# Optimization experiments

Hardware: AMD Instinct MI355X
Metric: run time of the kernel (lower is better)

Reference implementation:

```python
import jax, jax.numpy as jnp
import numpy as np


def setup_inputs() -> dict:
    key = jax.random.key(0)
    k1, k2, k3, k4 = jax.random.split(key, 4)
    B, T, K, N = 8, 16, 4096, 16384
    x = jax.random.normal(k1, (B, T, K), dtype=jnp.float32)
    # int8 weights in [-127, 127]
    weight_int8 = jax.random.randint(k2, (N, K), -127, 128, dtype=jnp.int32).astype(jnp.int8)
    # row-wise absmax scales (positive)
    weight_scales = jax.random.uniform(k3, (N,), dtype=jnp.float32, minval=0.1, maxval=2.0)
    bias = jax.random.normal(k4, (N,), dtype=jnp.float32)
    return {"x": x, "weight_int8": weight_int8, "weight_scales": weight_scales, "bias": bias}


def reference(x, weight_int8, weight_scales, bias):
    # dequantize_rowwise: W_fp = int8 * (scale / 127) per output row
    w = weight_int8.astype(x.dtype) * (weight_scales / 127.0).astype(x.dtype)[:, None]  # [N, K]
    # F.linear(x, w, bias) = x @ w.T + bias
    out = jnp.einsum('btk,nk->btn', x, w) + bias
    return out
```

## Files before the change

kernel.cpp:

```cpp
#include <hip/hip_runtime.h>
#include <hip/hip_bf16.h>

typedef __attribute__((ext_vector_type(8))) short short8;
typedef __attribute__((ext_vector_type(4))) float f32x4;
typedef __attribute__((ext_vector_type(4))) int   i32x4;

#define KD 4096
#define ND 16384
#define MD 128

__device__ __forceinline__ ushort f2bf_rn(float f) {
    unsigned u = __float_as_uint(f);
    u += 0x7FFFu + ((u >> 16) & 1u);
    return (ushort)(u >> 16);
}

__device__ __forceinline__ ushort i2bf(int v) {
    return (ushort)(__float_as_uint((float)v) >> 16);
}

__global__ __launch_bounds__(256) void pack_x_kernel(const float* __restrict__ x,
                                                     ushort* __restrict__ xp) {
    int tid  = blockIdx.x * 256 + threadIdx.x;
    int lane = tid & 63;
    int mt   = (tid >> 6) & 7;
    int kb   = tid >> 9;
    int m = (mt << 4) + (lane & 15);
    int k = (kb << 5) + ((lane >> 4) << 3);
    const f32x4* src = reinterpret_cast<const f32x4*>(x + (size_t)m * KD + k);
    f32x4 a = src[0];
    f32x4 b = src[1];
    short8 v;
    v[0] = (short)f2bf_rn(a[0]); v[1] = (short)f2bf_rn(a[1]);
    v[2] = (short)f2bf_rn(a[2]); v[3] = (short)f2bf_rn(a[3]);
    v[4] = (short)f2bf_rn(b[0]); v[5] = (short)f2bf_rn(b[1]);
    v[6] = (short)f2bf_rn(b[2]); v[7] = (short)f2bf_rn(b[3]);
    *reinterpret_cast<short8*>(xp + (size_t)tid * 8) = v;
}

#define GLOAD_LDS16(g, l)                                                        \
    __builtin_amdgcn_global_load_lds((const __attribute__((address_space(1))) void*)(g), \
                                     (__attribute__((address_space(3))) void*)(l), 16, 0, 0)

__global__ __launch_bounds__(512) void gemm_kernel(const int* __restrict__ wgt,
                                                   const ushort* __restrict__ xp,
                                                   const float* __restrict__ scales,
                                                   const float* __restrict__ bias,
                                                   float* __restrict__ out) {
    __shared__ __align__(16) char lds[98304];

    const int tid  = threadIdx.x;
    const int lane = tid & 63;
    const int w    = tid >> 6;
    const int n0   = blockIdx.x << 6;
    const int cl   = lane & 15;
    const int cq   = lane >> 4;

    if (w >= 4) {
        const int p = w - 4;
        const char* asrc = (const char*)xp + (p << 12) + (lane << 4);
        const int* wsrc0;
        const int* wsrc1;
        const int* wsrc2;
        const int* wsrc3;
        {
            int c0 = (p << 4) + 0  + cq;
            int c1 = (p << 4) + 4  + cq;
            int c2 = (p << 4) + 8  + cq;
            int c3 = (p << 4) + 12 + cq;
            wsrc0 = wgt + (size_t)(n0 + c0) * KD + ((cl ^ (c0 & 7)) << 2);
            wsrc1 = wgt + (size_t)(n0 + c1) * KD + ((cl ^ (c1 & 7)) << 2);
            wsrc2 = wgt + (size_t)(n0 + c2) * KD + ((cl ^ (c2 & 7)) << 2);
            wsrc3 = wgt + (size_t)(n0 + c3) * KD + ((cl ^ (c3 & 7)) << 2);
        }
        char* dA = lds + (p << 12);
        char* dW = lds + 49152 + (p << 12);

#define STAGE(t, b) do {                                                        \
            const char* _as = asrc + (size_t)(t) * 16384;                       \
            char* _dA = dA + (b) * 16384;                                       \
            GLOAD_LDS16(_as,        _dA);                                       \
            GLOAD_LDS16(_as + 1024, _dA + 1024);                                \
            GLOAD_LDS16(_as + 2048, _dA + 2048);                                \
            GLOAD_LDS16(_as + 3072, _dA + 3072);                                \
            const int _k0 = (t) * 64;                                           \
            char* _dW = dW + (b) * 16384;                                       \
            GLOAD_LDS16(wsrc0 + _k0, _dW);                                      \
            GLOAD_LDS16(wsrc1 + _k0, _dW + 1024);                               \
            GLOAD_LDS16(wsrc2 + _k0, _dW + 2048);                               \
            GLOAD_LDS16(wsrc3 + _k0, _dW + 3072);                               \
        } while (0)

        STAGE(0, 0);
        STAGE(1, 1);
        asm volatile("s_waitcnt vmcnt(8)" ::: "memory");
        __builtin_amdgcn_s_barrier();

        int b2 = 2;
#pragma unroll 1
        for (int t = 0; t < 64; ++t) {
            if (t + 2 < 64) {
                STAGE(t + 2, b2);
                asm volatile("s_waitcnt vmcnt(8)" ::: "memory");
            } else if (t + 1 < 64) {
                asm volatile("s_waitcnt vmcnt(0)" ::: "memory");
            }
            __builtin_amdgcn_s_barrier();
            b2 = (b2 == 2) ? 0 : b2 + 1;
        }
#undef STAGE
        return;
    }

    f32x4 acc[8];
#pragma unroll
    for (int i = 0; i < 8; ++i) acc[i] = (f32x4){0.f, 0.f, 0.f, 0.f};

    const char* rA = lds + (lane << 4);
    const char* rW = lds + 49152 + (((w << 4) + cl) << 8);
    const unsigned sw  = (unsigned)((cl & 7) << 4);
    const unsigned q32 = (unsigned)(cq << 5);

    __syncthreads();

    int bc = 0;
#pragma unroll 1
    for (int t = 0; t < 64; ++t) {
        const char* wb = rW + bc * 16384;
        const char* ab = rA + bc * 16384;
#pragma unroll
        for (int j = 0; j < 2; ++j) {
            unsigned off = (unsigned)((j << 7) + q32) ^ sw;
            i32x4 lo = *reinterpret_cast<const i32x4*>(wb + off);
            i32x4 hi = *reinterpret_cast<const i32x4*>(wb + (off ^ 16u));
            short8 bf;
            bf[0] = (short)i2bf(lo[0]); bf[1] = (short)i2bf(lo[1]);
            bf[2] = (short)i2bf(lo[2]); bf[3] = (short)i2bf(lo[3]);
            bf[4] = (short)i2bf(hi[0]); bf[5] = (short)i2bf(hi[1]);
            bf[6] = (short)i2bf(hi[2]); bf[7] = (short)i2bf(hi[3]);
            const char* aj = ab + j * 8192;
#pragma unroll
            for (int mt = 0; mt < 8; ++mt) {
                short8 af = *reinterpret_cast<const short8*>(aj + mt * 1024);
                acc[mt] = __builtin_amdgcn_mfma_f32_16x16x32_bf16(af, bf, acc[mt], 0, 0, 0);
            }
        }
        __syncthreads();
        bc = (bc == 2) ? 0 : bc + 1;
    }

    const int ncol = n0 + (w << 4) + cl;
    const float s  = scales[ncol] * (1.0f / 127.0f);
    const float bv = bias[ncol];
    const int rb = cq << 2;
#pragma unroll
    for (int mt = 0; mt < 8; ++mt) {
#pragma unroll
        for (int r = 0; r < 4; ++r) {
            int mg = (mt << 4) + rb + r;
            out[(size_t)mg * ND + ncol] = acc[mt][r] * s + bv;
        }
    }
}

extern "C" void kernel_launch(void* const* d_in, const int* in_sizes, int n_in,
                              void* d_out, int out_size, void* d_ws, size_t ws_size,
                              hipStream_t stream) {
    const float* x      = (const float*)d_in[0];
    const int*   wgt    = (const int*)d_in[1];
    const float* scales = (const float*)d_in[2];
    const float* bias   = (const float*)d_in[3];
    float* out = (float*)d_out;
    ushort* xp = (ushort*)d_ws;

    pack_x_kernel<<<MD * KD / (8 * 256), 256, 0, stream>>>(x, xp);
    gemm_kernel<<<256, 512, 0, stream>>>(wgt, xp, scales, bias, out);
}
```

Before: 57.77 us.

## Read activations directly from global memory and stage only weights through LDS

Producer waves now stage only weight tiles into LDS, using a K-tile twice as deep (128 ints per row, 32 iterations instead of 64) that fills the whole triple-buffered LDS region. Compute waves load the packed bf16 activation fragments straight from global memory, relying on the small activation buffer staying cache-resident. The aim is to halve producer load traffic and barrier count per K and give weight streaming the full LDS budget. In exchange, compute waves now wait on global or cache latency for activations with no prefetch, and the four compute waves each reload the same activation data.

```diff
diff --git a/kernel.cpp b/kernel.cpp
--- a/kernel.cpp
+++ b/kernel.cpp
@@ -58,37 +58,21 @@
 
     if (w >= 4) {
         const int p = w - 4;
-        const char* asrc = (const char*)xp + (p << 12) + (lane << 4);
-        const int* wsrc0;
-        const int* wsrc1;
-        const int* wsrc2;
-        const int* wsrc3;
-        {
-            int c0 = (p << 4) + 0  + cq;
-            int c1 = (p << 4) + 4  + cq;
-            int c2 = (p << 4) + 8  + cq;
-            int c3 = (p << 4) + 12 + cq;
-            wsrc0 = wgt + (size_t)(n0 + c0) * KD + ((cl ^ (c0 & 7)) << 2);
-            wsrc1 = wgt + (size_t)(n0 + c1) * KD + ((cl ^ (c1 & 7)) << 2);
-            wsrc2 = wgt + (size_t)(n0 + c2) * KD + ((cl ^ (c2 & 7)) << 2);
-            wsrc3 = wgt + (size_t)(n0 + c3) * KD + ((cl ^ (c3 & 7)) << 2);
+        const int* wsrc[8];
+#pragma unroll
+        for (int i = 0; i < 8; ++i) {
+            int c = (p << 4) + (i << 1) + (lane >> 5);
+            int k = ((lane & 31) << 2) ^ ((c & 7) << 2);
+            wsrc[i] = wgt + (size_t)(n0 + c) * KD + k;
         }
-        char* dA = lds + (p << 12);
-        char* dW = lds + 49152 + (p << 12);
+        char* dW = lds + (p << 13);
 
 #define STAGE(t, b) do {                                                        \
-            const char* _as = asrc + (size_t)(t) * 16384;                       \
-            char* _dA = dA + (b) * 16384;                                       \
-            GLOAD_LDS16(_as,        _dA);                                       \
-            GLOAD_LDS16(_as + 1024, _dA + 1024);                                \
-            GLOAD_LDS16(_as + 2048, _dA + 2048);                                \
-            GLOAD_LDS16(_as + 3072, _dA + 3072);                                \
-            const int _k0 = (t) * 64;                                           \
-            char* _dW = dW + (b) * 16384;                                       \
-            GLOAD_LDS16(wsrc0 + _k0, _dW);                                      \
-            GLOAD_LDS16(wsrc1 + _k0, _dW + 1024);                               \
-            GLOAD_LDS16(wsrc2 + _k0, _dW + 2048);                               \
-            GLOAD_LDS16(wsrc3 + _k0, _dW + 3072);                               \
+            const int _k0 = (t) * 128;                                          \
+            char* _d = dW + (b) * 32768;                                        \
+            _Pragma("unroll")                                                   \
+            for (int _i = 0; _i < 8; ++_i)                                      \
+                GLOAD_LDS16(wsrc[_i] + _k0, _d + _i * 1024);                    \
         } while (0)
 
         STAGE(0, 0);
@@ -98,11 +82,11 @@
 
         int b2 = 2;
 #pragma unroll 1
-        for (int t = 0; t < 64; ++t) {
-            if (t + 2 < 64) {
+        for (int t = 0; t < 32; ++t) {
+            if (t + 2 < 32) {
                 STAGE(t + 2, b2);
                 asm volatile("s_waitcnt vmcnt(8)" ::: "memory");
-            } else if (t + 1 < 64) {
+            } else if (t + 1 < 32) {
                 asm volatile("s_waitcnt vmcnt(0)" ::: "memory");
             }
             __builtin_amdgcn_s_barrier();
@@ -116,20 +100,25 @@
 #pragma unroll
     for (int i = 0; i < 8; ++i) acc[i] = (f32x4){0.f, 0.f, 0.f, 0.f};
 
-    const char* rA = lds + (lane << 4);
-    const char* rW = lds + 49152 + (((w << 4) + cl) << 8);
+    const char* rW = lds + (((w << 4) + cl) << 9);
     const unsigned sw  = (unsigned)((cl & 7) << 4);
     const unsigned q32 = (unsigned)(cq << 5);
+    const char* ax = (const char*)xp + (lane << 4);
 
     __syncthreads();
 
     int bc = 0;
 #pragma unroll 1
-    for (int t = 0; t < 64; ++t) {
-        const char* wb = rW + bc * 16384;
-        const char* ab = rA + bc * 16384;
+    for (int t = 0; t < 32; ++t) {
+        const char* wb = rW + bc * 32768;
+        const char* at = ax + (size_t)t * 32768;
 #pragma unroll
-        for (int j = 0; j < 2; ++j) {
+        for (int j = 0; j < 4; ++j) {
+            short8 af[8];
+            const char* aj = at + j * 8192;
+#pragma unroll
+            for (int mt = 0; mt < 8; ++mt)
+                af[mt] = *reinterpret_cast<const short8*>(aj + mt * 1024);
             unsigned off = (unsigned)((j << 7) + q32) ^ sw;
             i32x4 lo = *reinterpret_cast<const i32x4*>(wb + off);
             i32x4 hi = *reinterpret_cast<const i32x4*>(wb + (off ^ 16u));
@@ -138,12 +127,9 @@
             bf[2] = (short)i2bf(lo[2]); bf[3] = (short)i2bf(lo[3]);
             bf[4] = (short)i2bf(hi[0]); bf[5] = (short)i2bf(hi[1]);
             bf[6] = (short)i2bf(hi[2]); bf[7] = (short)i2bf(hi[3]);
-            const char* aj = ab + j * 8192;
 #pragma unroll
-            for (int mt = 0; mt < 8; ++mt) {
-                short8 af = *reinterpret_cast<const short8*>(aj + mt * 1024);
-                acc[mt] = __builtin_amdgcn_mfma_f32_16x16x32_bf16(af, bf, acc[mt], 0, 0, 0);
-            }
+            for (int mt = 0; mt < 8; ++mt)
+                acc[mt] = __builtin_amdgcn_mfma_f32_16x16x32_bf16(af[mt], bf, acc[mt], 0, 0, 0);
         }
         __syncthreads();
         bc = (bc == 2) ? 0 : bc + 1;
```

Result: slower. 87.16 us (+50.9%).

## Load weight tiles in 128-wide K chunks with separate double-buffered W pipeline

Applied to the files above, without the earlier changes.

Splits the producer staging into separate A and W loads: weights are now fetched 128 K-elements (512 B per row) at a time into a double-buffered 32 KB region, issued every other iteration, while activations remain triple-buffered per 64-K step. Wait counts are adjusted for the alternating issue pattern. The consumer indexes the W buffer by half-chunk offset. The aim is longer contiguous weight reads per row and fewer, larger load batches. The cost is more LDS (112 KB) and a more intricate wait-count schedule that could hurt overlap.

```diff
diff --git a/kernel.cpp b/kernel.cpp
--- a/kernel.cpp
+++ b/kernel.cpp
@@ -47,7 +47,7 @@
                                                    const float* __restrict__ scales,
                                                    const float* __restrict__ bias,
                                                    float* __restrict__ out) {
-    __shared__ __align__(16) char lds[98304];
+    __shared__ __align__(16) char lds[114688];
 
     const int tid  = threadIdx.x;
     const int lane = tid & 63;
@@ -59,56 +59,58 @@
     if (w >= 4) {
         const int p = w - 4;
         const char* asrc = (const char*)xp + (p << 12) + (lane << 4);
-        const int* wsrc0;
-        const int* wsrc1;
-        const int* wsrc2;
-        const int* wsrc3;
-        {
-            int c0 = (p << 4) + 0  + cq;
-            int c1 = (p << 4) + 4  + cq;
-            int c2 = (p << 4) + 8  + cq;
-            int c3 = (p << 4) + 12 + cq;
-            wsrc0 = wgt + (size_t)(n0 + c0) * KD + ((cl ^ (c0 & 7)) << 2);
-            wsrc1 = wgt + (size_t)(n0 + c1) * KD + ((cl ^ (c1 & 7)) << 2);
-            wsrc2 = wgt + (size_t)(n0 + c2) * KD + ((cl ^ (c2 & 7)) << 2);
-            wsrc3 = wgt + (size_t)(n0 + c3) * KD + ((cl ^ (c3 & 7)) << 2);
+        const int* wsrc[8];
+#pragma unroll
+        for (int i = 0; i < 8; ++i) {
+            int c = (p << 4) + (i << 1) + (lane >> 5);
+            int koff = (((lane & 31) ^ (c & 7)) << 2);
+            wsrc[i] = wgt + (size_t)(n0 + c) * KD + koff;
         }
         char* dA = lds + (p << 12);
-        char* dW = lds + 49152 + (p << 12);
+        char* dW = lds + 49152 + (p << 13);
 
-#define STAGE(t, b) do {                                                        \
-            const char* _as = asrc + (size_t)(t) * 16384;                       \
+#define STAGE_A(c, b) do {                                                      \
+            const char* _as = asrc + (size_t)(c) * 16384;                       \
             char* _dA = dA + (b) * 16384;                                       \
             GLOAD_LDS16(_as,        _dA);                                       \
             GLOAD_LDS16(_as + 1024, _dA + 1024);                                \
             GLOAD_LDS16(_as + 2048, _dA + 2048);                                \
             GLOAD_LDS16(_as + 3072, _dA + 3072);                                \
-            const int _k0 = (t) * 64;                                           \
-            char* _dW = dW + (b) * 16384;                                       \
-            GLOAD_LDS16(wsrc0 + _k0, _dW);                                      \
-            GLOAD_LDS16(wsrc1 + _k0, _dW + 1024);                               \
-            GLOAD_LDS16(wsrc2 + _k0, _dW + 2048);                               \
-            GLOAD_LDS16(wsrc3 + _k0, _dW + 3072);                               \
         } while (0)
 
-        STAGE(0, 0);
-        STAGE(1, 1);
-        asm volatile("s_waitcnt vmcnt(8)" ::: "memory");
+#define STAGE_W(u, b) do {                                                      \
+            const int _k0 = (u) * 128;                                          \
+            char* _dW = dW + (b) * 32768;                                       \
+            _Pragma("unroll")                                                   \
+            for (int _i = 0; _i < 8; ++_i)                                      \
+                GLOAD_LDS16(wsrc[_i] + _k0, _dW + _i * 1024);                   \
+        } while (0)
+
+        STAGE_A(0, 0);
+        STAGE_W(0, 0);
+        STAGE_A(1, 1);
+        asm volatile("s_waitcnt vmcnt(4)" ::: "memory");
         __builtin_amdgcn_s_barrier();
 
-        int b2 = 2;
+        int ba = 2;
 #pragma unroll 1
         for (int t = 0; t < 64; ++t) {
-            if (t + 2 < 64) {
-                STAGE(t + 2, b2);
-                asm volatile("s_waitcnt vmcnt(8)" ::: "memory");
-            } else if (t + 1 < 64) {
+            if (t < 62) {
+                STAGE_A(t + 2, ba);
+                if ((t & 1) == 0) STAGE_W((t >> 1) + 1, ((t >> 1) + 1) & 1);
+            }
+            if (t >= 62) {
                 asm volatile("s_waitcnt vmcnt(0)" ::: "memory");
+            } else if (t & 1) {
+                asm volatile("s_waitcnt vmcnt(4)" ::: "memory");
+            } else {
+                asm volatile("s_waitcnt vmcnt(12)" ::: "memory");
             }
             __builtin_amdgcn_s_barrier();
-            b2 = (b2 == 2) ? 0 : b2 + 1;
+            ba = (ba == 2) ? 0 : ba + 1;
         }
-#undef STAGE
+#undef STAGE_A
+#undef STAGE_W
         return;
     }
 
@@ -117,7 +119,7 @@
     for (int i = 0; i < 8; ++i) acc[i] = (f32x4){0.f, 0.f, 0.f, 0.f};
 
     const char* rA = lds + (lane << 4);
-    const char* rW = lds + 49152 + (((w << 4) + cl) << 8);
+    const char* rW = lds + 49152 + (((w << 4) + cl) << 9);
     const unsigned sw  = (unsigned)((cl & 7) << 4);
     const unsigned q32 = (unsigned)(cq << 5);
 
@@ -126,11 +128,12 @@
     int bc = 0;
 #pragma unroll 1
     for (int t = 0; t < 64; ++t) {
-        const char* wb = rW + bc * 16384;
+        const char* wb = rW + (((t >> 1) & 1) << 15);
+        const unsigned hoff = (unsigned)((t & 1) << 8);
         const char* ab = rA + bc * 16384;
 #pragma unroll
         for (int j = 0; j < 2; ++j) {
-            unsigned off = (unsigned)((j << 7) + q32) ^ sw;
+            unsigned off = (hoff + (unsigned)((j << 7) + q32)) ^ sw;
             i32x4 lo = *reinterpret_cast<const i32x4*>(wb + off);
             i32x4 hi = *reinterpret_cast<const i32x4*>(wb + (off ^ 16u));
             short8 bf;
```

New measurement: 59.49 us. 1.03x slower.
